# Performance work log

Hardware: AMD Instinct MI355X
Metric: run time of the kernel (lower is better)

## Reference

```python
import jax, jax.numpy as jnp
import numpy as np


def _neighbor_indices(H, W, r=10):
    # Faithful to init_neighbor_indices: for each pixel, the num_within_r nearest
    # pixels by Euclidean distance on the (H, W) grid (via argpartition).
    num = min(int(r * r * np.pi), H * W)  # 314 for r=10
    yy, xx = np.meshgrid(np.arange(H), np.arange(W), indexing='ij')
    fy, fx = yy.ravel(), xx.ravel()
    d2 = (fy[None, :] - fy[:, None]) ** 2 + (fx[None, :] - fx[:, None]) ** 2  # (I, I)
    idx = np.argpartition(d2, num, axis=1)[:, :num]  # (I, J)
    return idx.astype(np.int32)


def setup_inputs() -> dict:
    key = jax.random.key(0)
    ks = jax.random.split(key, 8)
    B, H, W, dim = 2, 48, 48, 64
    heads, dh, mult = 4, 8, 4
    inner = heads * dh            # 32
    hid = inner * mult // heads   # 32 per-head hidden channels
    n = H * W
    idx = jnp.asarray(_neighbor_indices(H, W, 10))
    s = lambda k, shp, sc: (jax.random.normal(k, shp, jnp.float32) * sc)
    return {
        'x': jax.random.normal(ks[0], (B, n, dim), jnp.float32),
        'idx': idx,                                   # (I, J) int32
        'w_qkv': s(ks[1], (dim, inner * 3), 0.08),    # Linear(dim, inner*3, bias=False)
        'w1': s(ks[2], (heads, hid, dh), 0.15),       # grouped 1x1 conv, per-head (out, in)
        'b1': s(ks[3], (heads, hid), 0.02),
        'w2': s(ks[4], (heads, dh, hid), 0.15),
        'b2': s(ks[5], (heads, dh), 0.02),
        'w_out': s(ks[6], (inner, dim), 0.1),         # Linear(inner, dim)
        'b_out': s(ks[7], (dim,), 0.02),
    }


def reference(x, idx, w_qkv, w1, b1, w2, b2, w_out, b_out):
    B, n, dim = x.shape
    h, hid, dh = w1.shape
    # qkv projection and head split: 'b n (h d) -> b h n d'
    q, k, v = jnp.split(x @ w_qkv, 3, axis=-1)
    sh = lambda t: t.reshape(B, n, h, dh).transpose(0, 2, 1, 3)  # (B,h,n,dh)
    q, k, v = sh(q), sh(k), sh(v)
    # neighbor gather (vector_select_batched_index): (B,h,I,J,dh)
    k1 = k[:, :, idx, :]
    v1 = v[:, :, idx, :]
    qk_rel = q[:, :, :, None, :] - k1                            # (B,h,I,J,dh)
    # attn_mlp: grouped 1x1 convs == per-head MLP over channel dim
    hmid = jax.nn.relu(jnp.einsum('bhijd,hed->bhije', qk_rel, w1)
                       + b1[None, :, None, None, :])
    sim = (jnp.einsum('bhije,hde->bhijd', hmid, w2)
           + b2[None, :, None, None, :])                        # (B,h,I,J,dh)
    # source softmaxes over dim=-2 of (B, h*dh, I, J), i.e. the pixel axis I
    attn = jax.nn.softmax(sim, axis=2)
    # einsum('b d i j, b i j d -> b i d') with channel d = (h dh)
    agg = jnp.einsum('bhijd,bhijd->bhid', attn, v1)              # (B,h,I,dh)
    agg = agg.transpose(0, 2, 1, 3).reshape(B, n, h * dh)
    return agg @ w_out + b_out
```

## Files before the change

kernel.cpp:

```cpp
#include <hip/hip_runtime.h>
#include <hip/hip_bf16.h>

#define BB 2
#define NH 4
#define NN 2304
#define DIM 64
#define DH 8
#define HID 32
#define KN 314

#define QKV_OFF 0
#define QKV_SZ  (BB*NN*96)
#define A_OFF   (QKV_OFF + QKV_SZ)
#define A_SZ    (BB*NH*NN*HID)
#define BK_OFF  (A_OFF + A_SZ)
#define BK_SZ   (BB*NH*NN*HID)
#define V_OFF   (BK_OFF + BK_SZ)
#define V_SZ    (BB*NH*NN*DH)
#define DEN_OFF (V_OFF + V_SZ)
#define DEN_SZ  (BB*NH*KN*DH)
#define AGG_OFF (DEN_OFF + DEN_SZ)
#define AGG_SZ  (BB*NH*NN*DH)
#define NUM_OFF (AGG_OFF + AGG_SZ)
#define NUM_ELTS ((size_t)BB*NH*NN*KN*DH)
#define BBF_OFF (NUM_OFF + NUM_ELTS/2)
#define WS_NEED_BYTES ((size_t)BBF_OFF*4 + (size_t)BK_SZ*2)

typedef float v2f __attribute__((ext_vector_type(2)));
typedef __attribute__((ext_vector_type(8))) short bf16x8;
typedef __attribute__((ext_vector_type(4))) float f32x4;
#define SWZ(x, imm) __int_as_float(__builtin_amdgcn_ds_swizzle(__float_as_int(x), imm))

static __device__ __forceinline__ float bfb(unsigned short u){
    return __uint_as_float(((unsigned)u) << 16);
}
static __device__ __forceinline__ unsigned cvtpk(float a, float b){
    unsigned r;
    asm("v_cvt_pk_bf16_f32 %0, %1, %2" : "=v"(r) : "v"(a), "v"(b));
    return r;
}
static __device__ __forceinline__ v2f unpk(unsigned u){
    v2f r; r.x = __uint_as_float(u << 16); r.y = __uint_as_float(u & 0xffff0000u); return r;
}
static __device__ __forceinline__ v2f mkv(float a, float b){ v2f r; r.x=a; r.y=b; return r; }

__global__ void qkv_kernel(const float* __restrict__ x, const float* __restrict__ w_qkv, float* ws){
    int t = blockIdx.x*256 + threadIdx.x;
    if (t >= BB*NN*96) return;
    int c = t % 96;
    int p = (t / 96) % NN;
    int b = t / (96*NN);
    const float* xr = x + (b*NN + p)*DIM;
    float acc = 0.f;
    #pragma unroll 8
    for (int dd=0; dd<DIM; dd++)
        acc = fmaf(xr[dd], w_qkv[dd*96 + c], acc);
    ws[QKV_OFF + (b*NN + p)*96 + c] = acc;
}

__global__ void ab_kernel(const float* __restrict__ w1, const float* __restrict__ b1, float* ws){
    int t = blockIdx.x*256 + threadIdx.x;
    if (t >= BB*NH*NN*HID) return;
    int e  = t % HID;
    int p  = (t / HID) % NN;
    int hh = (t / (HID*NN)) % NH;
    int b  = t / (HID*NN*NH);
    const float* qkv = ws + QKV_OFF + (b*NN + p)*96;
    const float* w1r = w1 + (hh*HID + e)*DH;
    float sa = b1[hh*HID + e];
    float sb = 0.f;
    #pragma unroll
    for (int d=0; d<DH; d++){
        float wv = w1r[d];
        sa = fmaf(wv, qkv[hh*DH + d],      sa);
        sb = fmaf(wv, qkv[32 + hh*DH + d], sb);
    }
    int base = ((b*NH + hh)*NN + p);
    ws[A_OFF  + base*HID + e] = sa;
    ws[BK_OFF + base*HID + e] = sb;
    ((unsigned short*)(ws + BBF_OFF))[(size_t)base*HID + e] = (unsigned short)cvtpk(sb, sb);
    if (e < DH)
        ws[V_OFF + base*DH + e] = qkv[64 + hh*DH + e];
}

__global__ __launch_bounds__(256) void pass1_mfma(const int* __restrict__ idx,
                                                  const float* __restrict__ w2,
                                                  const float* __restrict__ b2, float* ws){
    int lin = blockIdx.x + 20*(blockIdx.y + 16*blockIdx.z);
    int xcd = lin & 7, slot = lin >> 3;
    int fam = xcd*16 + slot/20;
    int jt  = slot - (slot/20)*20;
    int bh  = fam >> 4, yy = fam & 15;
    int hh  = bh & (NH-1);
    int w = threadIdx.x >> 6, lane = threadIdx.x & 63;
    int n  = lane & 15;
    int kg = lane >> 4;
    int strip = yy*4 + w;
    int i0 = strip*36;

    const float LG2E = 1.44269504088896340736f;
    float wv[8];
    #pragma unroll
    for (int tt=0; tt<8; tt++)
        wv[tt] = (n < DH) ? w2[(hh*DH + n)*HID + kg*8 + tt]*LG2E : 0.f;
    union { unsigned u[4]; bf16x8 v; } bfr;
    bfr.u[0] = cvtpk(wv[0], wv[1]);
    bfr.u[1] = cvtpk(wv[2], wv[3]);
    bfr.u[2] = cvtpk(wv[4], wv[5]);
    bfr.u[3] = cvtpk(wv[6], wv[7]);
    float b2v = (n < DH) ? b2[hh*DH + n]*LG2E : 0.f;
    f32x4 cinit; cinit[0]=b2v; cinit[1]=b2v; cinit[2]=b2v; cinit[3]=b2v;

    int jrow = jt*16 + n;
    int jj = jrow < KN ? jrow : (KN-1);
    int jr0 = jt*16 + kg*4;
    bool nok = (n < DH);
    bool st0 = nok && (jr0+0 < KN);
    bool st1 = nok && (jr0+1 < KN);
    bool st2 = nok && (jr0+2 < KN);
    bool st3 = nok && (jr0+3 < KN);

    const float* Abuf = ws + A_OFF + (size_t)bh*NN*HID;
    const unsigned short* Bbf = (const unsigned short*)(ws + BBF_OFF) + (size_t)bh*NN*HID;
    const int* idxp = idx + (size_t)i0*KN + jj;
    const float* ap = Abuf + (size_t)i0*HID + kg*8;

    unsigned short* numb = (unsigned short*)(ws + NUM_OFF);
    size_t nb = (((size_t)bh*NN + i0)*KN + jr0)*DH + (n & 7);
    const size_t NPI = (size_t)KN*DH;

    f32x4 den; den[0]=0.f; den[1]=0.f; den[2]=0.f; den[3]=0.f;

    int p0 = idxp[0], p1 = idxp[KN]; idxp += 2*KN;
    uint4 Bc0 = *(const uint4*)(Bbf + (size_t)p0*HID + kg*8);
    uint4 Bc1 = *(const uint4*)(Bbf + (size_t)p1*HID + kg*8);
    p0 = idxp[0]; p1 = idxp[KN]; idxp += 2*KN;

    for (int ii=0; ii<36; ii+=2){
        float4 a00 = *(const float4*)ap;
        float4 a01 = *(const float4*)(ap+4);
        float4 a10 = *(const float4*)(ap+HID);
        float4 a11 = *(const float4*)(ap+HID+4);
        ap += 2*HID;

        uint4 Bn0 = Bc0, Bn1 = Bc1;
        if (ii < 34){
            Bn0 = *(const uint4*)(Bbf + (size_t)p0*HID + kg*8);
            Bn1 = *(const uint4*)(Bbf + (size_t)p1*HID + kg*8);
        }
        if (ii < 32){ p0 = idxp[0]; p1 = idxp[KN]; idxp += 2*KN; }

        v2f r;
        union { unsigned u[4]; bf16x8 v; } af0, af1;
        r = mkv(a00.x, a00.y) - unpk(Bc0.x);
        af0.u[0] = cvtpk(fmaxf(r.x,0.f), fmaxf(r.y,0.f));
        r = mkv(a00.z, a00.w) - unpk(Bc0.y);
        af0.u[1] = cvtpk(fmaxf(r.x,0.f), fmaxf(r.y,0.f));
        r = mkv(a01.x, a01.y) - unpk(Bc0.z);
        af0.u[2] = cvtpk(fmaxf(r.x,0.f), fmaxf(r.y,0.f));
        r = mkv(a01.z, a01.w) - unpk(Bc0.w);
        af0.u[3] = cvtpk(fmaxf(r.x,0.f), fmaxf(r.y,0.f));
        r = mkv(a10.x, a10.y) - unpk(Bc1.x);
        af1.u[0] = cvtpk(fmaxf(r.x,0.f), fmaxf(r.y,0.f));
        r = mkv(a10.z, a10.w) - unpk(Bc1.y);
        af1.u[1] = cvtpk(fmaxf(r.x,0.f), fmaxf(r.y,0.f));
        r = mkv(a11.x, a11.y) - unpk(Bc1.z);
        af1.u[2] = cvtpk(fmaxf(r.x,0.f), fmaxf(r.y,0.f));
        r = mkv(a11.z, a11.w) - unpk(Bc1.w);
        af1.u[3] = cvtpk(fmaxf(r.x,0.f), fmaxf(r.y,0.f));

        f32x4 d0 = __builtin_amdgcn_mfma_f32_16x16x32_bf16(af0.v, bfr.v, cinit, 0, 0, 0);
        f32x4 d1 = __builtin_amdgcn_mfma_f32_16x16x32_bf16(af1.v, bfr.v, cinit, 0, 0, 0);

        float e00 = exp2f(d0[0]), e01 = exp2f(d0[1]), e02 = exp2f(d0[2]), e03 = exp2f(d0[3]);
        float e10 = exp2f(d1[0]), e11 = exp2f(d1[1]), e12 = exp2f(d1[2]), e13 = exp2f(d1[3]);
        den[0] += e00 + e10; den[1] += e01 + e11;
        den[2] += e02 + e12; den[3] += e03 + e13;

        unsigned u001 = cvtpk(e00, e01), u023 = cvtpk(e02, e03);
        unsigned u101 = cvtpk(e10, e11), u123 = cvtpk(e12, e13);
        if (st0){ numb[nb]        = (unsigned short)u001;
                  numb[nb + NPI]  = (unsigned short)u101; }
        if (st1){ numb[nb + DH]       = (unsigned short)(u001 >> 16);
                  numb[nb + NPI + DH] = (unsigned short)(u101 >> 16); }
        if (st2){ numb[nb + 2*DH]       = (unsigned short)u023;
                  numb[nb + NPI + 2*DH] = (unsigned short)u123; }
        if (st3){ numb[nb + 3*DH]       = (unsigned short)(u023 >> 16);
                  numb[nb + NPI + 3*DH] = (unsigned short)(u123 >> 16); }
        nb += 2*NPI;

        Bc0 = Bn0; Bc1 = Bn1;
    }

    if (nok){
        #pragma unroll
        for (int r2=0; r2<4; r2++){
            if (jr0 + r2 < KN)
                atomicAdd(ws + DEN_OFF + ((size_t)bh*KN + jr0 + r2)*DH + n, den[r2]);
        }
    }
}

__global__ void invden_kernel(float* ws){
    int t = blockIdx.x*256 + threadIdx.x;
    if (t < DEN_SZ){
        float* d = ws + DEN_OFF;
        d[t] = 1.0f / d[t];
    }
}

__global__ __launch_bounds__(256) void pass2f_kernel(const int* __restrict__ idx, float* ws){
    int hh = blockIdx.y, b = blockIdx.z;
    int w = threadIdx.x >> 6, lane = threadIdx.x & 63;
    int g = lane >> 3, dd = lane & 7;
    int bh = b*NH + hh;

    __shared__ float invs[KN*DH];
    {
        const float* den = ws + DEN_OFF + (size_t)bh*KN*DH;
        for (int t = threadIdx.x; t < KN*DH; t += 256) invs[t] = 1.0f / den[t];
    }
    __syncthreads();

    const float* Vbuf = ws + V_OFF + (size_t)bh*NN*DH;
    float* agg = ws + AGG_OFF + (size_t)bh*NN*DH;

    int i0 = blockIdx.x*8 + w*2;
    const unsigned short* num0 = (const unsigned short*)(ws + NUM_OFF)
                                 + ((size_t)bh*NN + i0)*KN*DH + dd;
    const unsigned short* num1 = num0 + (size_t)KN*DH;
    const int* ix0 = idx + (size_t)i0*KN;
    const int* ix1 = ix0 + KN;

    int p0 = ix0[g], p1 = ix1[g];
    float m0 = bfb(num0[g*DH]), m1 = bfb(num1[g*DH]);
    float acc0 = 0.f, acc1 = 0.f;

    for (int sg=0; sg<40; sg++){
        int jc = sg*8 + g;
        int jcc = jc < KN ? jc : (KN-1);
        float v0 = Vbuf[(size_t)p0*DH + dd];
        float v1 = Vbuf[(size_t)p1*DH + dd];
        float iv = invs[jcc*DH + dd];
        float w0 = m0 * iv, w1 = m1 * iv;
        if (jc >= KN){ w0 = 0.f; w1 = 0.f; }
        if (sg < 39){
            int jn = jc + 8; int jjn = jn < KN ? jn : (KN-1);
            p0 = ix0[jjn]; p1 = ix1[jjn];
            m0 = bfb(num0[(size_t)jjn*DH]);
            m1 = bfb(num1[(size_t)jjn*DH]);
        }
        acc0 = fmaf(w0, v0, acc0);
        acc1 = fmaf(w1, v1, acc1);
    }
    acc0 += __shfl_xor(acc0, 8, 64);
    acc0 += __shfl_xor(acc0, 16, 64);
    acc0 += __shfl_xor(acc0, 32, 64);
    acc1 += __shfl_xor(acc1, 8, 64);
    acc1 += __shfl_xor(acc1, 16, 64);
    acc1 += __shfl_xor(acc1, 32, 64);
    if (g == 0){
        agg[(size_t)i0*DH + dd]     = acc0;
        agg[(size_t)(i0+1)*DH + dd] = acc1;
    }
}

__device__ __forceinline__ void load_w2p(const float* __restrict__ w2, int hh, int dd,
                                         v2f w2a[8], v2f w2b[8]){
    #pragma unroll
    for (int m=0; m<8; m++){
        int d = dd ^ (((m&1)<<2) | (m&2) | ((m>>2)&1));
        const float* wp = w2 + (hh*DH + d)*HID + 4*dd;
        v2f a; a.x = wp[0]; a.y = wp[1];
        v2f b; b.x = wp[2]; b.y = wp[3];
        w2a[m] = a; w2b[m] = b;
    }
}
__device__ __forceinline__ float butterfly8p(float pr[8]){
    float q0 = pr[0] + SWZ(pr[4], 0x041F);
    float q1 = pr[1] + SWZ(pr[5], 0x041F);
    float q2 = pr[2] + SWZ(pr[6], 0x041F);
    float q3 = pr[3] + SWZ(pr[7], 0x041F);
    float r0 = q0 + SWZ(q2, 0x081F);
    float r1 = q1 + SWZ(q3, 0x081F);
    return r0 + SWZ(r1, 0x101F);
}
__global__ __launch_bounds__(256, 4) void pass1_small(const int* __restrict__ idx,
                                                      const float* __restrict__ w2,
                                                      const float* __restrict__ b2, float* ws){
    int sgic = blockIdx.x, hh = blockIdx.y, b = blockIdx.z;
    int sg = sgic >> 4, ic = sgic & 15;
    int w = threadIdx.x >> 6, lane = threadIdx.x & 63;
    int g = lane >> 3, dd = lane & 7;
    int j = sg*8 + g;
    bool jv = (j < KN);
    int jj = jv ? j : (KN-1);
    int bh = b*NH + hh;

    v2f w2a[8], w2b[8];
    load_w2p(w2, hh, dd, w2a, w2b);
    float b2v = b2[hh*DH + dd];

    const float* Abuf = ws + A_OFF  + (size_t)bh*NN*HID + 4*dd;
    const float* Bbuf = ws + BK_OFF + (size_t)bh*NN*HID + 4*dd;
    const int* idxc = idx + jj;

    float den_acc = 0.f;
    int i0 = ic*144 + w*36;
    for (int ii=0; ii<36; ii++){
        int i = i0 + ii;
        int p = idxc[(size_t)i*KN];
        float4 avv = *(const float4*)(Abuf + (size_t)i*HID);
        float4 bvv = *(const float4*)(Bbuf + (size_t)p*HID);
        v2f a0; a0.x=avv.x; a0.y=avv.y;
        v2f a1; a1.x=avv.z; a1.y=avv.w;
        v2f c0; c0.x=bvv.x; c0.y=bvv.y;
        v2f c1; c1.x=bvv.z; c1.y=bvv.w;
        v2f z;  z.x=0.f; z.y=0.f;
        v2f r0 = __builtin_elementwise_max(a0-c0, z);
        v2f r1 = __builtin_elementwise_max(a1-c1, z);
        float pr[8];
        #pragma unroll
        for (int m=0; m<8; m++){
            v2f t = w2a[m]*r0;
            t = __builtin_elementwise_fma(w2b[m], r1, t);
            pr[m] = t.x + t.y;
        }
        float sim = butterfly8p(pr) + b2v;
        den_acc += __expf(sim);
    }
    if (!jv) den_acc = 0.f;

    __shared__ float red[256];
    red[threadIdx.x] = den_acc;
    __syncthreads();
    if (w == 0 && jv){
        float s = red[lane] + red[lane+64] + red[lane+128] + red[lane+192];
        atomicAdd(ws + DEN_OFF + ((size_t)bh*KN + j)*DH + dd, s);
    }
}
__device__ __forceinline__ void load_w2s(const float* __restrict__ w2, int hh, int dd, float w2s[8][4]){
    #pragma unroll
    for (int m=0; m<8; m++){
        int d = ((m&1)<<2) | (m&2) | ((m>>2)&1);
        const float* wp = w2 + (hh*DH + d)*HID + 4*dd;
        w2s[m][0]=wp[0]; w2s[m][1]=wp[1]; w2s[m][2]=wp[2]; w2s[m][3]=wp[3];
    }
}
__device__ __forceinline__ float butterfly8(float pr[8], int dd){
    int b0 = dd&1, b1 = (dd>>1)&1, b2b = (dd>>2)&1;
    float q[4];
    #pragma unroll
    for (int t=0; t<4; t++){
        float send = pr[4*(1-b0)+t];
        float recv = __shfl_xor(send, 1, 64);
        q[t] = pr[4*b0+t] + recv;
    }
    float r[2];
    #pragma unroll
    for (int t=0; t<2; t++){
        float send = q[2*(1-b1)+t];
        float recv = __shfl_xor(send, 2, 64);
        r[t] = q[2*b1+t] + recv;
    }
    float send = r[1-b2b];
    float recv = __shfl_xor(send, 4, 64);
    return r[b2b] + recv;
}
__global__ __launch_bounds__(256) void pass2_kernel(const int* __restrict__ idx,
                                                    const float* __restrict__ w2,
                                                    const float* __restrict__ b2, float* ws){
    int ic = blockIdx.x, hh = blockIdx.y, b = blockIdx.z;
    int w = threadIdx.x >> 6, lane = threadIdx.x & 63;
    int g = lane >> 3, dd = lane & 7;

    float w2s[8][4];
    load_w2s(w2, hh, dd, w2s);
    float b2v = b2[hh*DH + dd];

    const float* Abuf = ws + A_OFF  + (size_t)(b*NH + hh)*NN*HID;
    const float* Bbuf = ws + BK_OFF + (size_t)(b*NH + hh)*NN*HID;
    const float* Vbuf = ws + V_OFF  + (size_t)(b*NH + hh)*NN*DH;
    const float* invd = ws + DEN_OFF + (size_t)(b*NH + hh)*KN*DH;
    float*       agg  = ws + AGG_OFF + (size_t)(b*NH + hh)*NN*DH;

    int i0 = ic*8 + w*2;
    #pragma unroll
    for (int ii=0; ii<2; ii++){
        int i = i0 + ii;
        float4 av = *(const float4*)(Abuf + (size_t)i*HID + 4*dd);
        float acc = 0.f;
        for (int sg=0; sg<40; sg++){
            int j = sg*8 + g;
            bool jvv = (j < KN);
            int jj = jvv ? j : (KN-1);
            int p = idx[i*KN + jj];
            float4 bv = *(const float4*)(Bbuf + (size_t)p*HID + 4*dd);
            float r0 = fmaxf(av.x-bv.x, 0.f), r1 = fmaxf(av.y-bv.y, 0.f);
            float r2 = fmaxf(av.z-bv.z, 0.f), r3 = fmaxf(av.w-bv.w, 0.f);
            float pr[8];
            #pragma unroll
            for (int m=0; m<8; m++)
                pr[m] = fmaf(w2s[m][0],r0, fmaf(w2s[m][1],r1, fmaf(w2s[m][2],r2, w2s[m][3]*r3)));
            float sim = butterfly8(pr, dd) + b2v;
            float attn = jvv ? (__expf(sim) * invd[(size_t)jj*DH + dd]) : 0.f;
            acc = fmaf(attn, Vbuf[(size_t)p*DH + dd], acc);
        }
        acc += __shfl_xor(acc, 8, 64);
        acc += __shfl_xor(acc, 16, 64);
        acc += __shfl_xor(acc, 32, 64);
        if (g == 0) agg[(size_t)i*DH + dd] = acc;
    }
}

__global__ void out_kernel(const float* __restrict__ w_out, const float* __restrict__ b_out,
                           const float* __restrict__ ws, float* __restrict__ out){
    int t = blockIdx.x*256 + threadIdx.x;
    if (t >= BB*NN*DIM) return;
    int c = t % DIM;
    int p = (t / DIM) % NN;
    int b = t / (DIM*NN);
    const float* agg = ws + AGG_OFF;
    float s = b_out[c];
    #pragma unroll
    for (int f=0; f<32; f++){
        int hh = f >> 3, d = f & 7;
        s = fmaf(agg[(((size_t)(b*NH + hh)*NN) + p)*DH + d], w_out[f*DIM + c], s);
    }
    out[t] = s;
}

extern "C" void kernel_launch(void* const* d_in, const int* in_sizes, int n_in,
                              void* d_out, int out_size, void* d_ws, size_t ws_size,
                              hipStream_t stream){
    const float* x     = (const float*)d_in[0];
    const int*   idx   = (const int*)d_in[1];
    const float* w_qkv = (const float*)d_in[2];
    const float* w1    = (const float*)d_in[3];
    const float* b1    = (const float*)d_in[4];
    const float* w2    = (const float*)d_in[5];
    const float* b2    = (const float*)d_in[6];
    const float* w_out = (const float*)d_in[7];
    const float* b_out = (const float*)d_in[8];
    float* ws  = (float*)d_ws;
    float* out = (float*)d_out;

    bool big = (ws_size >= WS_NEED_BYTES);

    hipMemsetAsync(ws + DEN_OFF, 0, DEN_SZ*sizeof(float), stream);

    qkv_kernel<<<(BB*NN*96 + 255)/256, 256, 0, stream>>>(x, w_qkv, ws);
    ab_kernel <<<(BB*NH*NN*HID + 255)/256, 256, 0, stream>>>(w1, b1, ws);
    if (big){
        pass1_mfma<<<dim3(20, 16, 8), 256, 0, stream>>>(idx, w2, b2, ws);
        pass2f_kernel<<<dim3(288, NH, BB), 256, 0, stream>>>(idx, ws);
    } else {
        pass1_small<<<dim3(640, NH, BB), 256, 0, stream>>>(idx, w2, b2, ws);
        invden_kernel<<<(DEN_SZ + 255)/256, 256, 0, stream>>>(ws);
        pass2_kernel<<<dim3(288, NH, BB), 256, 0, stream>>>(idx, w2, b2, ws);
    }
    out_kernel<<<(BB*NN*DIM + 255)/256, 256, 0, stream>>>(w_out, b_out, ws, out);
}
```

Before: 131.5 us.

## Transpose MFMA operands for vectorized numerator stores and rebalance pass1 grid

The pass1 MFMA now uses the weight fragment as the A operand and the activations as B, so each lane holds four consecutive output channels for one neighbor. The bf16 numerator can then be written with a single 8-byte store per row instead of four predicated 2-byte stores, and the bias init moves into per-lane channel values. Each strip now covers 48 pixels instead of 36, with a 20x12x8 grid and a simpler block-to-(bh, tile) mapping that drops the previous XCD-aware remap. Fewer, wider stores should cut write-transaction overhead, but half the lanes (kg>=2) now do wasted MFMA output work, and losing the XCD mapping may affect cache locality.

```diff
diff --git a/kernel.cpp b/kernel.cpp
--- a/kernel.cpp
+++ b/kernel.cpp
@@ -86,17 +86,17 @@
 __global__ __launch_bounds__(256) void pass1_mfma(const int* __restrict__ idx,
                                                   const float* __restrict__ w2,
                                                   const float* __restrict__ b2, float* ws){
-    int lin = blockIdx.x + 20*(blockIdx.y + 16*blockIdx.z);
-    int xcd = lin & 7, slot = lin >> 3;
-    int fam = xcd*16 + slot/20;
-    int jt  = slot - (slot/20)*20;
-    int bh  = fam >> 4, yy = fam & 15;
+    int lin = blockIdx.x + 20*(blockIdx.y + 12*blockIdx.z);
+    int bh  = lin & 7;
+    int rest = lin >> 3;
+    int jt  = rest % 20;
+    int yy  = rest / 20;
     int hh  = bh & (NH-1);
     int w = threadIdx.x >> 6, lane = threadIdx.x & 63;
     int n  = lane & 15;
     int kg = lane >> 4;
     int strip = yy*4 + w;
-    int i0 = strip*36;
+    int i0 = strip*48;
 
     const float LG2E = 1.44269504088896340736f;
     float wv[8];
@@ -108,17 +108,16 @@
     bfr.u[1] = cvtpk(wv[2], wv[3]);
     bfr.u[2] = cvtpk(wv[4], wv[5]);
     bfr.u[3] = cvtpk(wv[6], wv[7]);
-    float b2v = (n < DH) ? b2[hh*DH + n]*LG2E : 0.f;
-    f32x4 cinit; cinit[0]=b2v; cinit[1]=b2v; cinit[2]=b2v; cinit[3]=b2v;
+    f32x4 cinit;
+    #pragma unroll
+    for (int r=0; r<4; r++){
+        int d = kg*4 + r;
+        cinit[r] = (d < DH) ? b2[hh*DH + d]*LG2E : 0.f;
+    }
 
     int jrow = jt*16 + n;
     int jj = jrow < KN ? jrow : (KN-1);
-    int jr0 = jt*16 + kg*4;
-    bool nok = (n < DH);
-    bool st0 = nok && (jr0+0 < KN);
-    bool st1 = nok && (jr0+1 < KN);
-    bool st2 = nok && (jr0+2 < KN);
-    bool st3 = nok && (jr0+3 < KN);
+    bool stok = (jrow < KN) && (kg < 2);
 
     const float* Abuf = ws + A_OFF + (size_t)bh*NN*HID;
     const unsigned short* Bbf = (const unsigned short*)(ws + BBF_OFF) + (size_t)bh*NN*HID;
@@ -126,7 +125,7 @@
     const float* ap = Abuf + (size_t)i0*HID + kg*8;
 
     unsigned short* numb = (unsigned short*)(ws + NUM_OFF);
-    size_t nb = (((size_t)bh*NN + i0)*KN + jr0)*DH + (n & 7);
+    size_t nb = (((size_t)bh*NN + i0)*KN + jj)*DH + kg*4;
     const size_t NPI = (size_t)KN*DH;
 
     f32x4 den; den[0]=0.f; den[1]=0.f; den[2]=0.f; den[3]=0.f;
@@ -136,7 +135,7 @@
     uint4 Bc1 = *(const uint4*)(Bbf + (size_t)p1*HID + kg*8);
     p0 = idxp[0]; p1 = idxp[KN]; idxp += 2*KN;
 
-    for (int ii=0; ii<36; ii+=2){
+    for (int ii=0; ii<48; ii+=2){
         float4 a00 = *(const float4*)ap;
         float4 a01 = *(const float4*)(ap+4);
         float4 a10 = *(const float4*)(ap+HID);
@@ -144,11 +143,11 @@
         ap += 2*HID;
 
         uint4 Bn0 = Bc0, Bn1 = Bc1;
-        if (ii < 34){
+        if (ii < 46){
             Bn0 = *(const uint4*)(Bbf + (size_t)p0*HID + kg*8);
             Bn1 = *(const uint4*)(Bbf + (size_t)p1*HID + kg*8);
         }
-        if (ii < 32){ p0 = idxp[0]; p1 = idxp[KN]; idxp += 2*KN; }
+        if (ii < 44){ p0 = idxp[0]; p1 = idxp[KN]; idxp += 2*KN; }
 
         v2f r;
         union { unsigned u[4]; bf16x8 v; } af0, af1;
@@ -169,35 +168,30 @@
         r = mkv(a11.z, a11.w) - unpk(Bc1.w);
         af1.u[3] = cvtpk(fmaxf(r.x,0.f), fmaxf(r.y,0.f));
 
-        f32x4 d0 = __builtin_amdgcn_mfma_f32_16x16x32_bf16(af0.v, bfr.v, cinit, 0, 0, 0);
-        f32x4 d1 = __builtin_amdgcn_mfma_f32_16x16x32_bf16(af1.v, bfr.v, cinit, 0, 0, 0);
+        f32x4 d0 = __builtin_amdgcn_mfma_f32_16x16x32_bf16(bfr.v, af0.v, cinit, 0, 0, 0);
+        f32x4 d1 = __builtin_amdgcn_mfma_f32_16x16x32_bf16(bfr.v, af1.v, cinit, 0, 0, 0);
 
         float e00 = exp2f(d0[0]), e01 = exp2f(d0[1]), e02 = exp2f(d0[2]), e03 = exp2f(d0[3]);
         float e10 = exp2f(d1[0]), e11 = exp2f(d1[1]), e12 = exp2f(d1[2]), e13 = exp2f(d1[3]);
         den[0] += e00 + e10; den[1] += e01 + e11;
         den[2] += e02 + e12; den[3] += e03 + e13;
 
-        unsigned u001 = cvtpk(e00, e01), u023 = cvtpk(e02, e03);
-        unsigned u101 = cvtpk(e10, e11), u123 = cvtpk(e12, e13);
-        if (st0){ numb[nb]        = (unsigned short)u001;
-                  numb[nb + NPI]  = (unsigned short)u101; }
-        if (st1){ numb[nb + DH]       = (unsigned short)(u001 >> 16);
-                  numb[nb + NPI + DH] = (unsigned short)(u101 >> 16); }
-        if (st2){ numb[nb + 2*DH]       = (unsigned short)u023;
-                  numb[nb + NPI + 2*DH] = (unsigned short)u123; }
-        if (st3){ numb[nb + 3*DH]       = (unsigned short)(u023 >> 16);
-                  numb[nb + NPI + 3*DH] = (unsigned short)(u123 >> 16); }
+        if (stok){
+            uint2 s0; s0.x = cvtpk(e00, e01); s0.y = cvtpk(e02, e03);
+            uint2 s1; s1.x = cvtpk(e10, e11); s1.y = cvtpk(e12, e13);
+            *(uint2*)(numb + nb)       = s0;
+            *(uint2*)(numb + nb + NPI) = s1;
+        }
         nb += 2*NPI;
 
         Bc0 = Bn0; Bc1 = Bn1;
     }
 
-    if (nok){
+    if (stok){
+        float* denp = ws + DEN_OFF + ((size_t)bh*KN + jrow)*DH + kg*4;
         #pragma unroll
-        for (int r2=0; r2<4; r2++){
-            if (jr0 + r2 < KN)
-                atomicAdd(ws + DEN_OFF + ((size_t)bh*KN + jr0 + r2)*DH + n, den[r2]);
-        }
+        for (int r2=0; r2<4; r2++)
+            atomicAdd(denp + r2, den[r2]);
     }
 }
 
@@ -452,7 +446,7 @@
     qkv_kernel<<<(BB*NN*96 + 255)/256, 256, 0, stream>>>(x, w_qkv, ws);
     ab_kernel <<<(BB*NH*NN*HID + 255)/256, 256, 0, stream>>>(w1, b1, ws);
     if (big){
-        pass1_mfma<<<dim3(20, 16, 8), 256, 0, stream>>>(idx, w2, b2, ws);
+        pass1_mfma<<<dim3(20, 12, 8), 256, 0, stream>>>(idx, w2, b2, ws);
         pass2f_kernel<<<dim3(288, NH, BB), 256, 0, stream>>>(idx, ws);
     } else {
         pass1_small<<<dim3(640, NH, BB), 256, 0, stream>>>(idx, w2, b2, ws);
```

Result: faster. 127.7 us (-2.9%).
